# Kernel optimization log

Measured on AMD Instinct MI355X. Metric: run time of the kernel, lower is better.

## Reference

```python
import jax, jax.numpy as jnp
import numpy as np

B, T, D = 2, 2048, 2048
H, HKV, HD = 16, 4, 128
I = 5632
EPS = 1e-5


def setup_inputs() -> dict:
    ks = jax.random.split(jax.random.key(0), 12)
    s = 0.02
    return {
        "x": jax.random.normal(ks[0], (B, T, D), jnp.float32),
        "rope_cos": jax.random.uniform(ks[1], (T, HD // 2), jnp.float32),
        "rope_sin": jax.random.uniform(ks[2], (T, HD // 2), jnp.float32),
        "ln1_w": jnp.ones((D,), jnp.float32),
        "ln2_w": jnp.ones((D,), jnp.float32),
        "wq_w": jax.random.normal(ks[3], (D, H * HD), jnp.float32) * s,
        "wq_b": jnp.zeros((H * HD,), jnp.float32),
        "wk_w": jax.random.normal(ks[4], (D, HKV * HD), jnp.float32) * s,
        "wk_b": jnp.zeros((HKV * HD,), jnp.float32),
        "wv_w": jax.random.normal(ks[5], (D, HKV * HD), jnp.float32) * s,
        "wv_b": jnp.zeros((HKV * HD,), jnp.float32),
        "wo_w": jax.random.normal(ks[6], (H * HD, D), jnp.float32) * s,
        "wo_b": jnp.zeros((D,), jnp.float32),
        "w1_w": jax.random.normal(ks[7], (D, 2 * I), jnp.float32) * s,
        "w1_b": jnp.zeros((2 * I,), jnp.float32),
        "w2_w": jax.random.normal(ks[8], (I, D), jnp.float32) * s,
        "w2_b": jnp.zeros((D,), jnp.float32),
    }


def _rmsnorm(x, w):
    return x * jax.lax.rsqrt(jnp.mean(x * x, axis=-1, keepdims=True) + EPS) * w


def _rotate(x, cos, sin):
    # x: [B, h, T, HD]; cos/sin: [T, HD/2] broadcast over [B, h, T, HD/2]
    x1, x2 = x[..., ::2], x[..., 1::2]
    return jnp.stack([x1 * cos - x2 * sin, x1 * sin + x2 * cos], axis=-1).reshape(x.shape)


def reference(x, rope_cos, rope_sin, ln1_w, ln2_w, wq_w, wq_b, wk_w, wk_b,
              wv_w, wv_b, wo_w, wo_b, w1_w, w1_b, w2_w, w2_b):
    h = _rmsnorm(x, ln1_w)
    q = (h @ wq_w + wq_b).reshape(B, T, H, HD).transpose(0, 2, 1, 3)
    k = (h @ wk_w + wk_b).reshape(B, T, HKV, HD).transpose(0, 2, 1, 3)
    v = (h @ wv_w + wv_b).reshape(B, T, HKV, HD).transpose(0, 2, 1, 3)
    q = _rotate(q, rope_cos, rope_sin)
    k = _rotate(k, rope_cos, rope_sin)
    rep = H // HKV
    k = jnp.repeat(k, rep, axis=1)  # GQA repeat_interleave over head dim
    v = jnp.repeat(v, rep, axis=1)
    scale = 1.0 / np.sqrt(HD).astype(np.float32)
    scores = jnp.einsum('bhqd,bhkd->bhqk', q, k) * scale  # [B,H,T,T]
    causal = jnp.tril(jnp.ones((T, T), bool))
    scores = jnp.where(causal, scores, -jnp.inf)
    attn = jax.nn.softmax(scores, axis=-1)
    out = jnp.einsum('bhqk,bhkd->bhqd', attn, v)
    out = out.transpose(0, 2, 1, 3).reshape(B, T, H * HD) @ wo_w + wo_b
    h1 = x + out
    g = _rmsnorm(h1, ln2_w)
    gate_up = g @ w1_w + w1_b
    gate, up = gate_up[..., :I], gate_up[..., I:]
    mlp = (jax.nn.silu(gate) * up) @ w2_w + w2_b
    return h1 + mlp
```

## Files before the change

### kernel.cpp

```cpp
#include <hip/hip_runtime.h>

#define T_SEQ 2048
#define DMODEL 2048
#define NH 16
#define NKV 4
#define HD 128
#define ISZ 5632
#define BATCH 2
#define QKS 2560

typedef unsigned short ushort_t;
typedef __attribute__((ext_vector_type(8))) short short8;
typedef __attribute__((ext_vector_type(4))) float f32x4;

__device__ __forceinline__ ushort_t f2bf(float f) {
  unsigned int u = __float_as_uint(f);
  unsigned int r = (u + 0x7FFFu + ((u >> 16) & 1u)) >> 16;
  return (ushort_t)r;
}
__device__ __forceinline__ float bf2f(ushort_t h) {
  return __uint_as_float(((unsigned int)h) << 16);
}

__global__ __launch_bounds__(256) void wconv_kernel(const float* __restrict__ W,
                                                    ushort_t* __restrict__ Wt,
                                                    int K, int N) {
  __shared__ float tile[32][33];
  const int n0 = blockIdx.x * 32, k0 = blockIdx.y * 32;
  const int t = threadIdx.x;
  const int r = t >> 3, c = (t & 7) * 4;
  float4 v = *(const float4*)(W + (size_t)(k0 + r) * N + n0 + c);
  tile[r][c + 0] = v.x; tile[r][c + 1] = v.y; tile[r][c + 2] = v.z; tile[r][c + 3] = v.w;
  __syncthreads();
  ushort4 o;
  o.x = f2bf(tile[c + 0][r]);
  o.y = f2bf(tile[c + 1][r]);
  o.z = f2bf(tile[c + 2][r]);
  o.w = f2bf(tile[c + 3][r]);
  *(ushort4*)(Wt + (size_t)(n0 + r) * K + k0 + c) = o;
}

__global__ __launch_bounds__(256) void catbias_kernel(const float* __restrict__ a,
                                                      const float* __restrict__ b,
                                                      float* __restrict__ o) {
  int i = blockIdx.x * 256 + threadIdx.x;
  if (i < QKS) o[i] = (i < 2048) ? a[i] : b[i - 2048];
}

__global__ __launch_bounds__(256) void rmsnorm_kernel(const float* __restrict__ x,
                                                      const float* __restrict__ w,
                                                      ushort_t* __restrict__ out) {
  const int row = blockIdx.x;
  const int t = threadIdx.x;
  const float* xr = x + (size_t)row * DMODEL;
  float4 v0 = *(const float4*)(xr + t * 4);
  float4 v1 = *(const float4*)(xr + 1024 + t * 4);
  float ss = v0.x * v0.x + v0.y * v0.y + v0.z * v0.z + v0.w * v0.w +
             v1.x * v1.x + v1.y * v1.y + v1.z * v1.z + v1.w * v1.w;
  #pragma unroll
  for (int m = 1; m < 64; m <<= 1) ss += __shfl_xor(ss, m);
  __shared__ float red[4];
  if ((t & 63) == 0) red[t >> 6] = ss;
  __syncthreads();
  float tot = red[0] + red[1] + red[2] + red[3];
  float rinv = rsqrtf(tot * (1.0f / DMODEL) + 1e-5f);
  float4 w0 = *(const float4*)(w + t * 4);
  float4 w1 = *(const float4*)(w + 1024 + t * 4);
  ushort4 o0, o1;
  o0.x = f2bf(v0.x * rinv * w0.x); o0.y = f2bf(v0.y * rinv * w0.y);
  o0.z = f2bf(v0.z * rinv * w0.z); o0.w = f2bf(v0.w * rinv * w0.w);
  o1.x = f2bf(v1.x * rinv * w1.x); o1.y = f2bf(v1.y * rinv * w1.y);
  o1.z = f2bf(v1.z * rinv * w1.z); o1.w = f2bf(v1.w * rinv * w1.w);
  *(ushort4*)(out + (size_t)row * DMODEL + t * 4) = o0;
  *(ushort4*)(out + (size_t)row * DMODEL + 1024 + t * 4) = o1;
}

__global__ __launch_bounds__(256) void rope_kernel(ushort_t* __restrict__ buf,
                                                   const float* __restrict__ cs,
                                                   const float* __restrict__ sn) {
  size_t idx = (size_t)blockIdx.x * 256 + threadIdx.x;
  int d = (int)(idx & 63);
  size_t rest = idx >> 6;
  int hh = (int)(rest % 20);
  size_t bt = rest / 20;
  int t = (int)(bt & (T_SEQ - 1));
  ushort_t* p = buf + bt * QKS + hh * HD + 2 * d;
  float x1 = bf2f(p[0]), x2 = bf2f(p[1]);
  float c = cs[t * 64 + d], s = sn[t * 64 + d];
  p[0] = f2bf(x1 * c - x2 * s);
  p[1] = f2bf(x1 * s + x2 * c);
}

__global__ __launch_bounds__(256) void swiglu_kernel(ushort_t* __restrict__ gu) {
  size_t i = (size_t)blockIdx.x * 256 + threadIdx.x;
  size_t m = i / (ISZ / 8);
  size_t j = (i % (ISZ / 8)) * 8;
  ushort_t* pg = gu + m * (2 * ISZ) + j;
  short8 gg = *(const short8*)pg;
  short8 uu = *(const short8*)(pg + ISZ);
  short8 oo;
  #pragma unroll
  for (int q = 0; q < 8; ++q) {
    float gv = bf2f((ushort_t)gg[q]);
    float uv = bf2f((ushort_t)uu[q]);
    float sl = gv / (1.f + __expf(-gv));
    oo[q] = (short)f2bf(sl * uv);
  }
  *(short8*)pg = oo;
}

__global__ __launch_bounds__(512, 2)
void gemm256_kernel(const ushort_t* __restrict__ A, int lda,
                    const ushort_t* __restrict__ Bt,
                    const float* __restrict__ bias, void* __restrict__ outp,
                    int M, int N, int K) {
  __shared__ ushort_t lds[65536];
  const int tid = threadIdx.x;
  const int wid = tid >> 6, lane = tid & 63;
  const int lq = lane & 15, g = lane >> 4;
  const int wm = wid >> 2, wn = wid & 3;
  const int m0 = blockIdx.y * 256, n0 = blockIdx.x * 256;

  const char* ldsc = (const char*)lds;
  const int c0 = ((g ^ (lq & 3)) << 4) | (((lq >> 2) & 1) << 6);
  const int rbA = wm * 8192 + lq * 128 + c0;
  const int rbAx = rbA ^ 64;
  const int rbB = 32768 + wn * 4096 + lq * 128 + c0;
  const int rbBx = rbB ^ 64;

  const int l3 = lane >> 3;
  const int clog = ((lane & 7) ^ l3) << 4;
  const int s0 = wid * 16 + l3, s1 = s0 + 8;
  const int rA0 = (s0 & 63) + ((s0 >> 6) << 7);
  const int rA0b = (s1 & 63) + ((s1 >> 6) << 7);
  const int rB0 = ((s0 >> 5) << 6) + (s0 & 31);
  const int rB0b = ((s1 >> 5) << 6) + (s1 & 31);
  const char* pA0a = (const char*)A + (size_t)(m0 + rA0) * (lda * 2) + clog;
  const char* pA0b = (const char*)A + (size_t)(m0 + rA0b) * (lda * 2) + clog;
  const char* pA1a = pA0a + (size_t)64 * (lda * 2);
  const char* pA1b = pA0b + (size_t)64 * (lda * 2);
  const char* pB0a = (const char*)Bt + (size_t)(n0 + rB0) * (K * 2) + clog;
  const char* pB0b = (const char*)Bt + (size_t)(n0 + rB0b) * (K * 2) + clog;
  const char* pB1a = pB0a + (size_t)32 * (K * 2);
  const char* pB1b = pB0b + (size_t)32 * (K * 2);
  ushort_t* sd = lds + wid * 1024;

#define GLL(SRC, DOFF)                                                        \
  __builtin_amdgcn_global_load_lds(                                           \
      (const __attribute__((address_space(1))) void*)(SRC),                   \
      (__attribute__((address_space(3))) void*)(sd + (DOFF)), 16, 0, 0)
#define STG_ALL(PB)                                                           \
  {                                                                           \
    GLL(pA0a, (PB)*32768 + 0);     GLL(pA0b, (PB)*32768 + 512);               \
    GLL(pB0a, (PB)*32768 + 16384); GLL(pB0b, (PB)*32768 + 16896);             \
    GLL(pB1a, (PB)*32768 + 24576); GLL(pB1b, (PB)*32768 + 25088);             \
    GLL(pA1a, (PB)*32768 + 8192);  GLL(pA1b, (PB)*32768 + 8704);              \
    pA0a += 128; pA0b += 128; pA1a += 128; pA1b += 128;                       \
    pB0a += 128; pB0b += 128; pB1a += 128; pB1b += 128;                       \
  }

  f32x4 acc[8][4] = {};

#define TILE(P, DOST)                                                         \
  {                                                                           \
    asm volatile("s_waitcnt vmcnt(0)" ::: "memory");                          \
    __builtin_amdgcn_s_barrier();                                             \
    if (DOST) STG_ALL((P) ^ 1)                                                \
    short8 aA0[4][2], aA1[4][2], bb0[2][2], bb1[2][2];                        \
    _Pragma("unroll") for (int mi = 0; mi < 4; ++mi) {                        \
      aA0[mi][0] = *(const short8*)(ldsc + (P)*65536 + rbA + mi * 2048);      \
      aA0[mi][1] = *(const short8*)(ldsc + (P)*65536 + rbAx + mi * 2048);     \
    }                                                                         \
    _Pragma("unroll") for (int nj = 0; nj < 2; ++nj) {                        \
      bb0[nj][0] = *(const short8*)(ldsc + (P)*65536 + rbB + nj * 2048);      \
      bb0[nj][1] = *(const short8*)(ldsc + (P)*65536 + rbBx + nj * 2048);     \
    }                                                                         \
    _Pragma("unroll") for (int mi = 0; mi < 4; ++mi)                          \
      _Pragma("unroll") for (int nj = 0; nj < 2; ++nj) {                      \
        acc[mi][nj] = __builtin_amdgcn_mfma_f32_16x16x32_bf16(aA0[mi][0], bb0[nj][0], acc[mi][nj], 0, 0, 0); \
        acc[mi][nj] = __builtin_amdgcn_mfma_f32_16x16x32_bf16(aA0[mi][1], bb0[nj][1], acc[mi][nj], 0, 0, 0); \
      }                                                                       \
    _Pragma("unroll") for (int nj = 0; nj < 2; ++nj) {                        \
      bb1[nj][0] = *(const short8*)(ldsc + (P)*65536 + rbB + 16384 + nj * 2048);  \
      bb1[nj][1] = *(const short8*)(ldsc + (P)*65536 + rbBx + 16384 + nj * 2048); \
    }                                                                         \
    _Pragma("unroll") for (int mi = 0; mi < 4; ++mi)                          \
      _Pragma("unroll") for (int nj = 0; nj < 2; ++nj) {                      \
        acc[mi][2 + nj] = __builtin_amdgcn_mfma_f32_16x16x32_bf16(aA0[mi][0], bb1[nj][0], acc[mi][2 + nj], 0, 0, 0); \
        acc[mi][2 + nj] = __builtin_amdgcn_mfma_f32_16x16x32_bf16(aA0[mi][1], bb1[nj][1], acc[mi][2 + nj], 0, 0, 0); \
      }                                                                       \
    _Pragma("unroll") for (int mi = 0; mi < 4; ++mi) {                        \
      aA1[mi][0] = *(const short8*)(ldsc + (P)*65536 + rbA + 16384 + mi * 2048);  \
      aA1[mi][1] = *(const short8*)(ldsc + (P)*65536 + rbAx + 16384 + mi * 2048); \
    }                                                                         \
    _Pragma("unroll") for (int mi = 0; mi < 4; ++mi)                          \
      _Pragma("unroll") for (int nj = 0; nj < 2; ++nj) {                      \
        acc[4 + mi][nj] = __builtin_amdgcn_mfma_f32_16x16x32_bf16(aA1[mi][0], bb0[nj][0], acc[4 + mi][nj], 0, 0, 0); \
        acc[4 + mi][nj] = __builtin_amdgcn_mfma_f32_16x16x32_bf16(aA1[mi][1], bb0[nj][1], acc[4 + mi][nj], 0, 0, 0); \
      }                                                                       \
    _Pragma("unroll") for (int mi = 0; mi < 4; ++mi)                          \
      _Pragma("unroll") for (int nj = 0; nj < 2; ++nj) {                      \
        acc[4 + mi][2 + nj] = __builtin_amdgcn_mfma_f32_16x16x32_bf16(aA1[mi][0], bb1[nj][0], acc[4 + mi][2 + nj], 0, 0, 0); \
        acc[4 + mi][2 + nj] = __builtin_amdgcn_mfma_f32_16x16x32_bf16(aA1[mi][1], bb1[nj][1], acc[4 + mi][2 + nj], 0, 0, 0); \
      }                                                                       \
  }

  STG_ALL(0)
  for (int it = 0; it < 15; ++it) {
    TILE(0, true)
    TILE(1, true)
  }
  TILE(0, true)
  TILE(1, false)
#undef TILE
#undef GLL
#undef STG_ALL

  #pragma unroll
  for (int nf = 0; nf < 4; ++nf) {
    int c = n0 + wn * 64 + nf * 16 + lq;
    float bb = bias[c];
    #pragma unroll
    for (int mf = 0; mf < 8; ++mf) {
      #pragma unroll
      for (int i = 0; i < 4; ++i) {
        int r = m0 + wm * 128 + mf * 16 + g * 4 + i;
        ((ushort_t*)outp)[(size_t)r * N + c] = f2bf(acc[mf][nf][i] + bb);
      }
    }
  }
}

__global__ __launch_bounds__(512, 1)
void gemm128_kernel(const ushort_t* __restrict__ A, int lda,
                    const ushort_t* __restrict__ Bt,
                    const float* __restrict__ bias, const float* __restrict__ res,
                    float* __restrict__ outp, int M, int N, int K) {
  __shared__ ushort_t lds[49152];
  const int tid = threadIdx.x;
  const int wid = tid >> 6, lane = tid & 63;
  const int lq = lane & 15, g = lane >> 4;
  const int wm = wid & 1, wn = wid >> 1;
  const int m0 = blockIdx.y * 128, n0 = blockIdx.x * 256;
  const int NT = K >> 6;

  const char* ldsc = (const char*)lds;
  const int c0 = ((g ^ (lq & 3)) << 4) | (((lq >> 2) & 1) << 6);
  const int rbA = wm * 8192 + lq * 128 + c0;
  const int rbAx = rbA ^ 64;
  const int rbB = 16384 + wn * 8192 + lq * 128 + c0;
  const int rbBx = rbB ^ 64;

  const char* pA[2];
  const char* pB[4];
  #pragma unroll
  for (int j = 0; j < 2; ++j) {
    int pb = (wid * 2 + j) * 1024 + lane * 16;
    int ob = pb ^ (((pb >> 7) & 7) << 4);
    pA[j] = (const char*)A + (size_t)(m0 + (ob >> 7)) * (lda * 2) + (ob & 127);
  }
  #pragma unroll
  for (int j = 0; j < 4; ++j) {
    int pb = (wid * 4 + j) * 1024 + lane * 16;
    int ob = pb ^ (((pb >> 7) & 7) << 4);
    pB[j] = (const char*)Bt + (size_t)(n0 + (ob >> 7)) * (K * 2) + (ob & 127);
  }
  ushort_t* sdA = lds + wid * 1024;
  ushort_t* sdB = lds + 8192 + wid * 2048;

#define GLL1(SRC, DST)                                                        \
  __builtin_amdgcn_global_load_lds(                                           \
      (const __attribute__((address_space(1))) void*)(SRC),                   \
      (__attribute__((address_space(3))) void*)(DST), 16, 0, 0)
#define STG128(PB)                                                            \
  {                                                                           \
    GLL1(pA[0], sdA + (PB)*24576 + 0);   GLL1(pA[1], sdA + (PB)*24576 + 512); \
    GLL1(pB[0], sdB + (PB)*24576 + 0);   GLL1(pB[1], sdB + (PB)*24576 + 512); \
    GLL1(pB[2], sdB + (PB)*24576 + 1024); GLL1(pB[3], sdB + (PB)*24576 + 1536); \
    pA[0] += 128; pA[1] += 128;                                               \
    pB[0] += 128; pB[1] += 128; pB[2] += 128; pB[3] += 128;                   \
  }

  f32x4 acc[4][4] = {};

#define TILE128(P, TCUR)                                                      \
  {                                                                           \
    asm volatile("s_waitcnt vmcnt(0)" ::: "memory");                          \
    __builtin_amdgcn_s_barrier();                                             \
    if ((TCUR) + 1 < NT) STG128((P) ^ 1)                                      \
    short8 aA[4][2], bb[4][2];                                                \
    _Pragma("unroll") for (int mi = 0; mi < 4; ++mi) {                        \
      aA[mi][0] = *(const short8*)(ldsc + (P)*49152 + rbA + mi * 2048);       \
      aA[mi][1] = *(const short8*)(ldsc + (P)*49152 + rbAx + mi * 2048);      \
    }                                                                         \
    _Pragma("unroll") for (int nj = 0; nj < 4; ++nj) {                        \
      bb[nj][0] = *(const short8*)(ldsc + (P)*49152 + rbB + nj * 2048);       \
      bb[nj][1] = *(const short8*)(ldsc + (P)*49152 + rbBx + nj * 2048);      \
    }                                                                         \
    _Pragma("unroll") for (int mi = 0; mi < 4; ++mi)                          \
      _Pragma("unroll") for (int nj = 0; nj < 4; ++nj) {                      \
        acc[mi][nj] = __builtin_amdgcn_mfma_f32_16x16x32_bf16(aA[mi][0], bb[nj][0], acc[mi][nj], 0, 0, 0); \
        acc[mi][nj] = __builtin_amdgcn_mfma_f32_16x16x32_bf16(aA[mi][1], bb[nj][1], acc[mi][nj], 0, 0, 0); \
      }                                                                       \
  }

  STG128(0)
  for (int t = 0; t < NT; t += 2) {
    TILE128(0, t)
    TILE128(1, t + 1)
  }
#undef TILE128
#undef GLL1
#undef STG128

  #pragma unroll
  for (int nf = 0; nf < 4; ++nf) {
    int c = n0 + wn * 64 + nf * 16 + lq;
    float bb = bias[c];
    #pragma unroll
    for (int mf = 0; mf < 4; ++mf) {
      #pragma unroll
      for (int i = 0; i < 4; ++i) {
        int r = m0 + wm * 64 + mf * 16 + g * 4 + i;
        size_t oidx = (size_t)r * N + c;
        outp[oidx] = res[oidx] + acc[mf][nf][i] + bb;
      }
    }
  }
}

#define BM 128
#define BN 128
#define BK 32

template <int MODE>
__global__ __launch_bounds__(256, 2)
void gemm_kernel(const ushort_t* __restrict__ A, int lda, const ushort_t* __restrict__ Bt,
                 const float* __restrict__ bias, const float* __restrict__ res,
                 void* __restrict__ outp, int M, int N, int K) {
  __shared__ ushort_t Alds[BM * BK];
  __shared__ ushort_t Blds[BM * BK];
  const int tid = threadIdx.x;
  const int w = tid >> 6, lane = tid & 63;
  const int lq = lane & 15, g = lane >> 4;
  const int m0 = blockIdx.y * BM, n0 = blockIdx.x * BN;
  const int ro = (w >> 1) * 64, co = (w & 1) * 64;

  f32x4 acc[4][4] = {};

  for (int k0 = 0; k0 < K; k0 += BK) {
    const ushort_t* ga = A + (size_t)m0 * lda + k0;
    const ushort_t* gb = Bt + (size_t)n0 * K + k0;
    #pragma unroll
    for (int it = 0; it < 2; ++it) {
      int ch = it * 256 + tid;
      int row = ch >> 2, cir = ch & 3;
      int lbase = (it * 256 + w * 64) * 8;
      __builtin_amdgcn_global_load_lds(
          (const __attribute__((address_space(1))) void*)(ga + (size_t)row * lda + cir * 8),
          (__attribute__((address_space(3))) void*)(&Alds[lbase]), 16, 0, 0);
      __builtin_amdgcn_global_load_lds(
          (const __attribute__((address_space(1))) void*)(gb + (size_t)row * K + cir * 8),
          (__attribute__((address_space(3))) void*)(&Blds[lbase]), 16, 0, 0);
    }
    __syncthreads();
    short8 af[4], br[4];
    #pragma unroll
    for (int mi = 0; mi < 4; ++mi)
      af[mi] = *(const short8*)(&Alds[(ro + mi * 16 + lq) * BK + g * 8]);
    #pragma unroll
    for (int ni = 0; ni < 4; ++ni)
      br[ni] = *(const short8*)(&Blds[(co + ni * 16 + lq) * BK + g * 8]);
    #pragma unroll
    for (int mi = 0; mi < 4; ++mi)
      #pragma unroll
      for (int ni = 0; ni < 4; ++ni)
        acc[mi][ni] = __builtin_amdgcn_mfma_f32_16x16x32_bf16(af[mi], br[ni], acc[mi][ni], 0, 0, 0);
    __syncthreads();
  }

  #pragma unroll
  for (int ni = 0; ni < 4; ++ni) {
    int c = n0 + co + ni * 16 + lq;
    float bb = bias[c];
    #pragma unroll
    for (int mi = 0; mi < 4; ++mi) {
      #pragma unroll
      for (int i = 0; i < 4; ++i) {
        int r = m0 + ro + mi * 16 + g * 4 + i;
        size_t oidx = (size_t)r * N + c;
        float av = acc[mi][ni][i] + bb;
        if (MODE == 1) {
          ((float*)outp)[oidx] = res[oidx] + av;
        } else {
          int b2 = r >> 11, t2 = r & (T_SEQ - 1);
          int hk = c >> 7, dd = c & (HD - 1);
          ((ushort_t*)outp)[((size_t)(b2 * NKV + hk) * HD + dd) * T_SEQ + t2] = f2bf(av);
        }
      }
    }
  }
}

#define QB 64
#define KB 64
#define KSTR 136
#define VSTR 72
#define PSTR 72

__global__ __launch_bounds__(256, 2)
void attn_kernel(const ushort_t* __restrict__ qk, const ushort_t* __restrict__ vT,
                 ushort_t* __restrict__ ao) {
  __shared__ ushort_t Klds[KB * KSTR];
  __shared__ ushort_t Vlds[HD * VSTR];
  __shared__ ushort_t Plds[4][16 * PSTR];

  const int tid = threadIdx.x;
  const int w = tid >> 6, lane = tid & 63;
  const int lq = lane & 15, g = lane >> 4;
  const int nqb = T_SEQ / QB;
  const int xq = blockIdx.x;
  const int qi = (xq & 1) ? (nqb - 1 - (xq >> 1)) : (xq >> 1);
  const int qb = qi * QB;
  const int h = blockIdx.y;
  const int b = blockIdx.z;
  const int hkv = h >> 2;
  const int qw = qb + w * 16;
  const float scale = 0.08838834764831845f;

  short8 qf[4];
  {
    const ushort_t* qrow = qk + ((size_t)(b * T_SEQ + qw + lq) * QKS) + h * HD;
    #pragma unroll
    for (int ks = 0; ks < 4; ++ks) qf[ks] = *(const short8*)(qrow + ks * 32 + g * 8);
  }

  f32x4 of[8] = {};
  float m_run = -1e30f, l_run = 0.f;

  const ushort_t* kbase = qk + (size_t)b * T_SEQ * QKS + 2048 + hkv * HD;
  const ushort_t* vbase = vT + (size_t)(b * NKV + hkv) * HD * T_SEQ;

  const int nt = (qb + QB) / KB;
  for (int ti = 0; ti < nt; ++ti) {
    const int kt = ti * KB;
    #pragma unroll
    for (int it = 0; it < 4; ++it) {
      int ch = it * 256 + tid;
      int krow = ch >> 4, kdk = (ch & 15) * 8;
      *(short8*)(&Klds[krow * KSTR + kdk]) =
          *(const short8*)(kbase + (size_t)(kt + krow) * QKS + kdk);
      int vd = ch >> 3, vj = (ch & 7) * 8;
      *(short8*)(&Vlds[vd * VSTR + vj]) =
          *(const short8*)(vbase + (size_t)vd * T_SEQ + kt + vj);
    }
    __syncthreads();
    if (kt <= qw + 15) {
      f32x4 s[4] = {};
      __builtin_amdgcn_s_setprio(1);
      #pragma unroll
      for (int c = 0; c < 4; ++c)
        #pragma unroll
        for (int ks = 0; ks < 4; ++ks) {
          short8 kf = *(const short8*)(&Klds[(c * 16 + lq) * KSTR + ks * 32 + g * 8]);
          s[c] = __builtin_amdgcn_mfma_f32_16x16x32_bf16(kf, qf[ks], s[c], 0, 0, 0);
        }
      __builtin_amdgcn_s_setprio(0);
      const int qg = qw + lq;
      float sv[16];
      #pragma unroll
      for (int c = 0; c < 4; ++c)
        #pragma unroll
        for (int i = 0; i < 4; ++i) {
          int kvg = kt + c * 16 + 4 * g + i;
          float xx = s[c][i] * scale;
          sv[c * 4 + i] = (kvg > qg) ? -1e30f : xx;
        }
      float tmax = sv[0];
      #pragma unroll
      for (int j = 1; j < 16; ++j) tmax = fmaxf(tmax, sv[j]);
      tmax = fmaxf(tmax, __shfl_xor(tmax, 16));
      tmax = fmaxf(tmax, __shfl_xor(tmax, 32));
      float mnew = fmaxf(m_run, tmax);
      float corr = __expf(m_run - mnew);
      float pv[16];
      float ps = 0.f;
      #pragma unroll
      for (int j = 0; j < 16; ++j) { pv[j] = __expf(sv[j] - mnew); ps += pv[j]; }
      ps += __shfl_xor(ps, 16);
      ps += __shfl_xor(ps, 32);
      l_run = l_run * corr + ps;
      m_run = mnew;
      float c4[4];
      #pragma unroll
      for (int i = 0; i < 4; ++i) c4[i] = __shfl(corr, 4 * g + i);
      #pragma unroll
      for (int n = 0; n < 8; ++n)
        #pragma unroll
        for (int i = 0; i < 4; ++i) of[n][i] *= c4[i];
      #pragma unroll
      for (int c = 0; c < 4; ++c) {
        ushort4 pw;
        pw.x = f2bf(pv[c * 4 + 0]); pw.y = f2bf(pv[c * 4 + 1]);
        pw.z = f2bf(pv[c * 4 + 2]); pw.w = f2bf(pv[c * 4 + 3]);
        *(ushort4*)(&Plds[w][lq * PSTR + c * 16 + 4 * g]) = pw;
      }
      short8 pf0 = *(const short8*)(&Plds[w][lq * PSTR + g * 8]);
      short8 pf1 = *(const short8*)(&Plds[w][lq * PSTR + 32 + g * 8]);
      __builtin_amdgcn_s_setprio(1);
      #pragma unroll
      for (int n = 0; n < 8; ++n) {
        short8 vf0 = *(const short8*)(&Vlds[(n * 16 + lq) * VSTR + g * 8]);
        short8 vf1 = *(const short8*)(&Vlds[(n * 16 + lq) * VSTR + 32 + g * 8]);
        of[n] = __builtin_amdgcn_mfma_f32_16x16x32_bf16(pf0, vf0, of[n], 0, 0, 0);
        of[n] = __builtin_amdgcn_mfma_f32_16x16x32_bf16(pf1, vf1, of[n], 0, 0, 0);
      }
      __builtin_amdgcn_s_setprio(0);
    }
    __syncthreads();
  }
  float li[4];
  #pragma unroll
  for (int i = 0; i < 4; ++i) li[i] = 1.f / __shfl(l_run, 4 * g + i);
  #pragma unroll
  for (int n = 0; n < 8; ++n)
    #pragma unroll
    for (int i = 0; i < 4; ++i) {
      int tok = qw + 4 * g + i;
      ao[((size_t)(b * T_SEQ + tok) * (NH * HD)) + h * HD + n * 16 + lq] = f2bf(of[n][i] * li[i]);
    }
}

extern "C" void kernel_launch(void* const* d_in, const int* in_sizes, int n_in,
                              void* d_out, int out_size, void* d_ws, size_t ws_size,
                              hipStream_t stream) {
  const float* x   = (const float*)d_in[0];
  const float* rc  = (const float*)d_in[1];
  const float* rs  = (const float*)d_in[2];
  const float* ln1 = (const float*)d_in[3];
  const float* ln2 = (const float*)d_in[4];
  const float* wq  = (const float*)d_in[5];
  const float* wqb = (const float*)d_in[6];
  const float* wk  = (const float*)d_in[7];
  const float* wkb = (const float*)d_in[8];
  const float* wv  = (const float*)d_in[9];
  const float* wvb = (const float*)d_in[10];
  const float* wo  = (const float*)d_in[11];
  const float* wob = (const float*)d_in[12];
  const float* w1  = (const float*)d_in[13];
  const float* w1b = (const float*)d_in[14];
  const float* w2  = (const float*)d_in[15];
  const float* w2b = (const float*)d_in[16];

  char* ws = (char*)d_ws;
  size_t off = 0;
  auto alloc = [&](size_t bytes) {
    char* p = ws + off;
    off += (bytes + 255) & ~(size_t)255;
    return (void*)p;
  };
  const int M = BATCH * T_SEQ;
  ushort_t* w1T  = (ushort_t*)alloc((size_t)11264 * 2048 * 2);
  ushort_t* w2T  = (ushort_t*)alloc((size_t)2048 * 5632 * 2);
  ushort_t* hbuf = (ushort_t*)alloc((size_t)M * 2048 * 2);
  ushort_t* vbufT= (ushort_t*)alloc((size_t)M * 512 * 2);
  float*    qkb  = (float*)alloc((size_t)QKS * 4);
  size_t guStart = off;
  ushort_t* wqkT = (ushort_t*)alloc((size_t)QKS * 2048 * 2);
  ushort_t* wvT  = (ushort_t*)alloc((size_t)512 * 2048 * 2);
  ushort_t* woT  = (ushort_t*)alloc((size_t)2048 * 2048 * 2);
  ushort_t* qkbuf= (ushort_t*)alloc((size_t)M * QKS * 2);
  size_t guBytes = (size_t)M * 11264 * 2;
  size_t used = off - guStart;
  if (guBytes > used) alloc(guBytes - used);
  ushort_t* gu = (ushort_t*)(ws + guStart);
  float* h1 = (float*)d_out;
  if (off > ws_size) return;

  wconv_kernel<<<dim3(2048 / 32, 2048 / 32), 256, 0, stream>>>(wq, wqkT, 2048, 2048);
  wconv_kernel<<<dim3(512 / 32, 2048 / 32), 256, 0, stream>>>(wk, wqkT + (size_t)2048 * 2048, 2048, 512);
  wconv_kernel<<<dim3(512 / 32, 2048 / 32), 256, 0, stream>>>(wv, wvT, 2048, 512);
  wconv_kernel<<<dim3(2048 / 32, 2048 / 32), 256, 0, stream>>>(wo, woT, 2048, 2048);
  wconv_kernel<<<dim3(11264 / 32, 2048 / 32), 256, 0, stream>>>(w1, w1T, 2048, 11264);
  wconv_kernel<<<dim3(2048 / 32, 5632 / 32), 256, 0, stream>>>(w2, w2T, 5632, 2048);
  catbias_kernel<<<10, 256, 0, stream>>>(wqb, wkb, qkb);

  rmsnorm_kernel<<<M, 256, 0, stream>>>(x, ln1, hbuf);

  gemm256_kernel<<<dim3(QKS / 256, M / 256), 512, 0, stream>>>(hbuf, 2048, wqkT, qkb, qkbuf, M, QKS, 2048);
  gemm_kernel<3><<<dim3(512 / BN, M / BM), 256, 0, stream>>>(hbuf, 2048, wvT, wvb, nullptr, vbufT, M, 512, 2048);

  rope_kernel<<<(M * 20 * 64) / 256, 256, 0, stream>>>(qkbuf, rc, rs);

  attn_kernel<<<dim3(T_SEQ / QB, NH, BATCH), 256, 0, stream>>>(qkbuf, vbufT, hbuf);

  gemm128_kernel<<<dim3(2048 / 256, M / 128), 512, 0, stream>>>(hbuf, 2048, woT, wob, x, h1, M, 2048, 2048);

  rmsnorm_kernel<<<M, 256, 0, stream>>>(h1, ln2, hbuf);

  gemm256_kernel<<<dim3(11264 / 256, M / 256), 512, 0, stream>>>(hbuf, 2048, w1T, w1b, gu, M, 11264, 2048);

  swiglu_kernel<<<(M * (ISZ / 8)) / 256, 256, 0, stream>>>(gu);

  gemm128_kernel<<<dim3(2048 / 256, M / 128), 512, 0, stream>>>(gu, 11264, w2T, w2b, h1, (float*)d_out, M, 2048, 5632);

  (void)in_sizes; (void)n_in; (void)out_size;
}
```

Baseline: 700.8 us.

## Double attention query tile and load K/V directly into swizzled LDS

```diff
diff --git a/kernel.cpp b/kernel.cpp
--- a/kernel.cpp
+++ b/kernel.cpp
@@ -402,17 +402,15 @@
   }
 }
 
-#define QB 64
+#define QB 128
 #define KB 64
-#define KSTR 136
-#define VSTR 72
 #define PSTR 72
 
 __global__ __launch_bounds__(256, 2)
 void attn_kernel(const ushort_t* __restrict__ qk, const ushort_t* __restrict__ vT,
                  ushort_t* __restrict__ ao) {
-  __shared__ ushort_t Klds[KB * KSTR];
-  __shared__ ushort_t Vlds[HD * VSTR];
+  __shared__ ushort_t Klds[KB * 128];
+  __shared__ ushort_t Vlds[HD * 64];
   __shared__ ushort_t Plds[4][16 * PSTR];
 
   const int tid = threadIdx.x;
@@ -425,110 +423,142 @@
   const int h = blockIdx.y;
   const int b = blockIdx.z;
   const int hkv = h >> 2;
-  const int qw = qb + w * 16;
   const float scale = 0.08838834764831845f;
 
-  short8 qf[4];
-  {
-    const ushort_t* qrow = qk + ((size_t)(b * T_SEQ + qw + lq) * QKS) + h * HD;
-    #pragma unroll
-    for (int ks = 0; ks < 4; ++ks) qf[ks] = *(const short8*)(qrow + ks * 32 + g * 8);
-  }
-
-  f32x4 of[8] = {};
-  float m_run = -1e30f, l_run = 0.f;
-
-  const ushort_t* kbase = qk + (size_t)b * T_SEQ * QKS + 2048 + hkv * HD;
-  const ushort_t* vbase = vT + (size_t)(b * NKV + hkv) * HD * T_SEQ;
-
-  const int nt = (qb + QB) / KB;
+  short8 qf[2][4];
+  #pragma unroll
+  for (int gi = 0; gi < 2; ++gi) {
+    const ushort_t* qrow = qk + ((size_t)(b * T_SEQ + qb + gi * 64 + w * 16 + lq) * QKS) + h * HD;
+    #pragma unroll
+    for (int ks = 0; ks < 4; ++ks) qf[gi][ks] = *(const short8*)(qrow + ks * 32 + g * 8);
+  }
+
+  f32x4 of[2][8] = {};
+  float m_run[2] = {-1e30f, -1e30f};
+  float l_run[2] = {0.f, 0.f};
+
+  const char* kbaseC = (const char*)(qk + (size_t)b * T_SEQ * QKS + 2048 + hkv * HD);
+  const char* vbaseC = (const char*)(vT + (size_t)(b * NKV + hkv) * HD * T_SEQ);
+  const char* pK[4];
+  const char* pV[4];
+  #pragma unroll
+  for (int j = 0; j < 4; ++j) {
+    int krow = w * 16 + j * 4 + (lane >> 4);
+    int kcol = ((lane & 15) * 16) ^ ((krow & 7) << 4);
+    pK[j] = kbaseC + (size_t)krow * (QKS * 2) + kcol;
+    int vrow = w * 32 + j * 8 + (lane >> 3);
+    int vcol = ((lane & 7) * 16) ^ ((vrow & 7) << 4);
+    pV[j] = vbaseC + (size_t)vrow * (T_SEQ * 2) + vcol;
+  }
+  ushort_t* kdst = Klds + w * 2048;
+  ushort_t* vdst = Vlds + w * 2048;
+  const char* kldsC = (const char*)Klds;
+  const char* vldsC = (const char*)Vlds;
+
+#define AGLL(SRC, DST)                                                        \
+  __builtin_amdgcn_global_load_lds(                                           \
+      (const __attribute__((address_space(1))) void*)(SRC),                   \
+      (__attribute__((address_space(3))) void*)(DST), 16, 0, 0)
+
+  const int nt = qb / KB + 2;
   for (int ti = 0; ti < nt; ++ti) {
     const int kt = ti * KB;
     #pragma unroll
-    for (int it = 0; it < 4; ++it) {
-      int ch = it * 256 + tid;
-      int krow = ch >> 4, kdk = (ch & 15) * 8;
-      *(short8*)(&Klds[krow * KSTR + kdk]) =
-          *(const short8*)(kbase + (size_t)(kt + krow) * QKS + kdk);
-      int vd = ch >> 3, vj = (ch & 7) * 8;
-      *(short8*)(&Vlds[vd * VSTR + vj]) =
-          *(const short8*)(vbase + (size_t)vd * T_SEQ + kt + vj);
+    for (int j = 0; j < 4; ++j) {
+      AGLL(pK[j], kdst + j * 512);
+      AGLL(pV[j], vdst + j * 512);
+      pK[j] += (size_t)KB * (QKS * 2);
+      pV[j] += KB * 2;
     }
-    __syncthreads();
-    if (kt <= qw + 15) {
-      f32x4 s[4] = {};
-      __builtin_amdgcn_s_setprio(1);
+    asm volatile("s_waitcnt vmcnt(0)" ::: "memory");
+    __builtin_amdgcn_s_barrier();
+
+    #pragma unroll
+    for (int gi = 0; gi < 2; ++gi) {
+      const int qw = qb + gi * 64 + w * 16;
+      if (kt <= qw + 15) {
+        f32x4 s[4] = {};
+        __builtin_amdgcn_s_setprio(1);
+        #pragma unroll
+        for (int c = 0; c < 4; ++c) {
+          int krow = c * 16 + lq;
+          #pragma unroll
+          for (int ks = 0; ks < 4; ++ks) {
+            short8 kf = *(const short8*)(kldsC + krow * 256 + (((ks * 64) + g * 16) ^ ((krow & 7) << 4)));
+            s[c] = __builtin_amdgcn_mfma_f32_16x16x32_bf16(kf, qf[gi][ks], s[c], 0, 0, 0);
+          }
+        }
+        __builtin_amdgcn_s_setprio(0);
+        const int qg = qw + lq;
+        float sv[16];
+        #pragma unroll
+        for (int c = 0; c < 4; ++c)
+          #pragma unroll
+          for (int i = 0; i < 4; ++i) {
+            int kvg = kt + c * 16 + 4 * g + i;
+            float xx = s[c][i] * scale;
+            sv[c * 4 + i] = (kvg > qg) ? -1e30f : xx;
+          }
+        float tmax = sv[0];
+        #pragma unroll
+        for (int j = 1; j < 16; ++j) tmax = fmaxf(tmax, sv[j]);
+        tmax = fmaxf(tmax, __shfl_xor(tmax, 16));
+        tmax = fmaxf(tmax, __shfl_xor(tmax, 32));
+        float mnew = fmaxf(m_run[gi], tmax);
+        float corr = __expf(m_run[gi] - mnew);
+        float pv[16];
+        float ps = 0.f;
+        #pragma unroll
+        for (int j = 0; j < 16; ++j) { pv[j] = __expf(sv[j] - mnew); ps += pv[j]; }
+        ps += __shfl_xor(ps, 16);
+        ps += __shfl_xor(ps, 32);
+        l_run[gi] = l_run[gi] * corr + ps;
+        m_run[gi] = mnew;
+        float c4[4];
+        #pragma unroll
+        for (int i = 0; i < 4; ++i) c4[i] = __shfl(corr, 4 * g + i);
+        #pragma unroll
+        for (int n = 0; n < 8; ++n)
+          #pragma unroll
+          for (int i = 0; i < 4; ++i) of[gi][n][i] *= c4[i];
+        #pragma unroll
+        for (int c = 0; c < 4; ++c) {
+          ushort4 pw;
+          pw.x = f2bf(pv[c * 4 + 0]); pw.y = f2bf(pv[c * 4 + 1]);
+          pw.z = f2bf(pv[c * 4 + 2]); pw.w = f2bf(pv[c * 4 + 3]);
+          *(ushort4*)(&Plds[w][lq * PSTR + c * 16 + 4 * g]) = pw;
+        }
+        short8 pf0 = *(const short8*)(&Plds[w][lq * PSTR + g * 8]);
+        short8 pf1 = *(const short8*)(&Plds[w][lq * PSTR + 32 + g * 8]);
+        __builtin_amdgcn_s_setprio(1);
+        #pragma unroll
+        for (int n = 0; n < 8; ++n) {
+          int vr = n * 16 + lq;
+          short8 vf0 = *(const short8*)(vldsC + vr * 128 + ((g * 16) ^ ((vr & 7) << 4)));
+          short8 vf1 = *(const short8*)(vldsC + vr * 128 + ((64 + g * 16) ^ ((vr & 7) << 4)));
+          of[gi][n] = __builtin_amdgcn_mfma_f32_16x16x32_bf16(pf0, vf0, of[gi][n], 0, 0, 0);
+          of[gi][n] = __builtin_amdgcn_mfma_f32_16x16x32_bf16(pf1, vf1, of[gi][n], 0, 0, 0);
+        }
+        __builtin_amdgcn_s_setprio(0);
+      }
+    }
+    __builtin_amdgcn_s_barrier();
+  }
+#undef AGLL
+
+  #pragma unroll
+  for (int gi = 0; gi < 2; ++gi) {
+    float li[4];
+    #pragma unroll
+    for (int i = 0; i < 4; ++i) li[i] = 1.f / __shfl(l_run[gi], 4 * g + i);
+    #pragma unroll
+    for (int n = 0; n < 8; ++n)
       #pragma unroll
-      for (int c = 0; c < 4; ++c)
-        #pragma unroll
-        for (int ks = 0; ks < 4; ++ks) {
-          short8 kf = *(const short8*)(&Klds[(c * 16 + lq) * KSTR + ks * 32 + g * 8]);
-          s[c] = __builtin_amdgcn_mfma_f32_16x16x32_bf16(kf, qf[ks], s[c], 0, 0, 0);
-        }
-      __builtin_amdgcn_s_setprio(0);
-      const int qg = qw + lq;
-      float sv[16];
-      #pragma unroll
-      for (int c = 0; c < 4; ++c)
-        #pragma unroll
-        for (int i = 0; i < 4; ++i) {
-          int kvg = kt + c * 16 + 4 * g + i;
-          float xx = s[c][i] * scale;
-          sv[c * 4 + i] = (kvg > qg) ? -1e30f : xx;
-        }
-      float tmax = sv[0];
-      #pragma unroll
-      for (int j = 1; j < 16; ++j) tmax = fmaxf(tmax, sv[j]);
-      tmax = fmaxf(tmax, __shfl_xor(tmax, 16));
-      tmax = fmaxf(tmax, __shfl_xor(tmax, 32));
-      float mnew = fmaxf(m_run, tmax);
-      float corr = __expf(m_run - mnew);
-      float pv[16];
-      float ps = 0.f;
-      #pragma unroll
-      for (int j = 0; j < 16; ++j) { pv[j] = __expf(sv[j] - mnew); ps += pv[j]; }
-      ps += __shfl_xor(ps, 16);
-      ps += __shfl_xor(ps, 32);
-      l_run = l_run * corr + ps;
-      m_run = mnew;
-      float c4[4];
-      #pragma unroll
-      for (int i = 0; i < 4; ++i) c4[i] = __shfl(corr, 4 * g + i);
-      #pragma unroll
-      for (int n = 0; n < 8; ++n)
-        #pragma unroll
-        for (int i = 0; i < 4; ++i) of[n][i] *= c4[i];
-      #pragma unroll
-      for (int c = 0; c < 4; ++c) {
-        ushort4 pw;
-        pw.x = f2bf(pv[c * 4 + 0]); pw.y = f2bf(pv[c * 4 + 1]);
-        pw.z = f2bf(pv[c * 4 + 2]); pw.w = f2bf(pv[c * 4 + 3]);
-        *(ushort4*)(&Plds[w][lq * PSTR + c * 16 + 4 * g]) = pw;
+      for (int i = 0; i < 4; ++i) {
+        int tok = qb + gi * 64 + w * 16 + 4 * g + i;
+        ao[((size_t)(b * T_SEQ + tok) * (NH * HD)) + h * HD + n * 16 + lq] = f2bf(of[gi][n][i] * li[i]);
       }
-      short8 pf0 = *(const short8*)(&Plds[w][lq * PSTR + g * 8]);
-      short8 pf1 = *(const short8*)(&Plds[w][lq * PSTR + 32 + g * 8]);
-      __builtin_amdgcn_s_setprio(1);
-      #pragma unroll
-      for (int n = 0; n < 8; ++n) {
-        short8 vf0 = *(const short8*)(&Vlds[(n * 16 + lq) * VSTR + g * 8]);
-        short8 vf1 = *(const short8*)(&Vlds[(n * 16 + lq) * VSTR + 32 + g * 8]);
-        of[n] = __builtin_amdgcn_mfma_f32_16x16x32_bf16(pf0, vf0, of[n], 0, 0, 0);
-        of[n] = __builtin_amdgcn_mfma_f32_16x16x32_bf16(pf1, vf1, of[n], 0, 0, 0);
-      }
-      __builtin_amdgcn_s_setprio(0);
-    }
-    __syncthreads();
-  }
-  float li[4];
-  #pragma unroll
-  for (int i = 0; i < 4; ++i) li[i] = 1.f / __shfl(l_run, 4 * g + i);
-  #pragma unroll
-  for (int n = 0; n < 8; ++n)
-    #pragma unroll
-    for (int i = 0; i < 4; ++i) {
-      int tok = qw + 4 * g + i;
-      ao[((size_t)(b * T_SEQ + tok) * (NH * HD)) + h * HD + n * 16 + lq] = f2bf(of[n][i] * li[i]);
-    }
+  }
 }
 
 extern "C" void kernel_launch(void* const* d_in, const int* in_sizes, int n_in,
```

Measured after the change: 694.3 us. Within noise of the previous version (-0.9%).
